# Kernel tuning notes

Measured on AMD Instinct MI355X. Metric: run time of the kernel, lower is better.

Reference implementation:

```python
import jax, jax.numpy as jnp
import numpy as np

N_NODES = 150000
N_USERS = 100000
EMB = 64
N_EDGES = 4800000
N_LAYERS = 3


def setup_inputs() -> dict:
    key = jax.random.key(0)
    k1, k2, k3, k4 = jax.random.split(key, 4)
    emb_weight = jax.random.normal(k1, (N_NODES, EMB), dtype=jnp.float32)
    adj_row = jnp.sort(jax.random.randint(k2, (N_EDGES,), 0, N_NODES, dtype=jnp.int64))
    adj_col = jax.random.randint(k3, (N_EDGES,), 0, N_NODES, dtype=jnp.int64)
    adj_vals = jax.random.uniform(k4, (N_EDGES,), dtype=jnp.float32)
    return {
        "emb_weight": emb_weight,
        "adj_row": adj_row,
        "adj_col": adj_col,
        "adj_vals": adj_vals,
        "n_users": N_USERS,
        "n_nodes": N_NODES,
        "n_layers": N_LAYERS,
    }


def _spmm(row, col, vals, x, n_nodes):
    # COO SpMM: out[r] += vals[e] * x[col[e]]  for each edge e with row[e]==r
    gathered = x[col] * vals[:, None]            # [nnz, emb]
    return jax.ops.segment_sum(gathered, row, num_segments=n_nodes)


def reference(emb_weight, adj_row, adj_col, adj_vals, n_users, n_nodes, n_layers):
    all_emb = emb_weight
    embs_sum = all_emb                           # running sum instead of stack+mean
    for _ in range(n_layers):
        all_emb = _spmm(adj_row, adj_col, adj_vals, all_emb, n_nodes)
        embs_sum = embs_sum + all_emb
    final_emb = embs_sum / jnp.asarray(n_layers + 1, dtype=emb_weight.dtype)
    users = final_emb[:n_users]
    items = final_emb[n_users:]
    return (users, items)
```

## Files before the change

### kernel.cpp

```cpp
#include <hip/hip_runtime.h>

#define EMB 64

__device__ __forceinline__ float bl(unsigned int u) { return __uint_as_float(u << 16); }
__device__ __forceinline__ float bh(unsigned int u) { return __uint_as_float(u & 0xffff0000u); }
__device__ __forceinline__ unsigned int pack2(float a, float b) {
    unsigned int ua = __float_as_uint(a); ua += 0x7fffu + ((ua >> 16) & 1u);
    unsigned int ub = __float_as_uint(b); ub += 0x7fffu + ((ub >> 16) & 1u);
    return (ua >> 16) | (ub & 0xffff0000u);
}

__global__ void __launch_bounds__(256) k_rowptr(const int* __restrict__ row,
                                                int* __restrict__ ptr, int E, int R) {
    int e = blockIdx.x * blockDim.x + threadIdx.x;
    if (e >= E) return;
    int r = row[e];
    int prev = (e == 0) ? -1 : row[e - 1];
    for (int q = prev + 1; q <= r; ++q) ptr[q] = e;
    if (e == E - 1) {
        for (int q = r + 1; q <= R; ++q) ptr[q] = E;
    }
}

__global__ void __launch_bounds__(256) k_prep(const float* __restrict__ emb,
                                              uint4* __restrict__ Xb, int n8) {
    int i = blockIdx.x * blockDim.x + threadIdx.x;
    if (i >= n8) return;
    const float4* p = reinterpret_cast<const float4*>(emb) + (size_t)i * 2;
    float4 a = p[0], b = p[1];
    uint4 x;
    x.x = pack2(a.x, a.y); x.y = pack2(a.z, a.w);
    x.z = pack2(b.x, b.y); x.w = pack2(b.z, b.w);
    Xb[i] = x;
}

template <int FINAL>
__global__ void __launch_bounds__(256, 3) k_spmm(const int* __restrict__ ptr,
                                                 const int* __restrict__ col,
                                                 const float* __restrict__ vals,
                                                 const uint4* __restrict__ Xb,
                                                 uint4* __restrict__ Yb,
                                                 const float* __restrict__ emb,
                                                 const uint4* __restrict__ Xa,
                                                 const uint4* __restrict__ Xc,
                                                 float* __restrict__ out, int R) {
    int tid = blockIdx.x * blockDim.x + threadIdx.x;
    int g   = tid >> 3;
    int gl  = tid & 7;
    if (g >= R) return;

    int s = ptr[g];
    int e = ptr[g + 1];

    float acc0 = 0.f, acc1 = 0.f, acc2 = 0.f, acc3 = 0.f;
    float acc4 = 0.f, acc5 = 0.f, acc6 = 0.f, acc7 = 0.f;

    if (s < e) {
        for (int base = s; base < e; base += 16) {
            int   cv[16];
            float vv[16];
            #pragma unroll
            for (int j = 0; j < 16; ++j) {
                int idx = base + j;
                int i2  = idx < e ? idx : e - 1;
                cv[j] = col[i2];
                vv[j] = vals[i2];
            }
            uint4 xv[16];
            #pragma unroll
            for (int j = 0; j < 16; ++j)
                xv[j] = Xb[(size_t)((unsigned)cv[j] * 8u + (unsigned)gl)];
            #pragma unroll
            for (int j = 0; j < 16; ++j) {
                float v = (base + j < e) ? vv[j] : 0.f;
                acc0 = fmaf(v, bl(xv[j].x), acc0);
                acc1 = fmaf(v, bh(xv[j].x), acc1);
                acc2 = fmaf(v, bl(xv[j].y), acc2);
                acc3 = fmaf(v, bh(xv[j].y), acc3);
                acc4 = fmaf(v, bl(xv[j].z), acc4);
                acc5 = fmaf(v, bh(xv[j].z), acc5);
                acc6 = fmaf(v, bl(xv[j].w), acc6);
                acc7 = fmaf(v, bh(xv[j].w), acc7);
            }
        }
    }

    if (FINAL) {
        const float4* er = reinterpret_cast<const float4*>(emb + (size_t)g * EMB + gl * 8);
        float4 a = er[0], b = er[1];
        uint4 x1 = Xa[(size_t)g * 8 + gl];
        uint4 x2 = Xc[(size_t)g * 8 + gl];
        float4 o0, o1;
        o0.x = 0.25f * (a.x + bl(x1.x) + bl(x2.x) + acc0);
        o0.y = 0.25f * (a.y + bh(x1.x) + bh(x2.x) + acc1);
        o0.z = 0.25f * (a.z + bl(x1.y) + bl(x2.y) + acc2);
        o0.w = 0.25f * (a.w + bh(x1.y) + bh(x2.y) + acc3);
        o1.x = 0.25f * (b.x + bl(x1.z) + bl(x2.z) + acc4);
        o1.y = 0.25f * (b.y + bh(x1.z) + bh(x2.z) + acc5);
        o1.z = 0.25f * (b.z + bl(x1.w) + bl(x2.w) + acc6);
        o1.w = 0.25f * (b.w + bh(x1.w) + bh(x2.w) + acc7);
        float4* q = reinterpret_cast<float4*>(out + (size_t)g * EMB + gl * 8);
        q[0] = o0; q[1] = o1;
    } else {
        uint4 y;
        y.x = pack2(acc0, acc1); y.y = pack2(acc2, acc3);
        y.z = pack2(acc4, acc5); y.w = pack2(acc6, acc7);
        Yb[(size_t)g * 8 + gl] = y;
    }
}

extern "C" void kernel_launch(void* const* d_in, const int* in_sizes, int n_in,
                              void* d_out, int out_size, void* d_ws, size_t ws_size,
                              hipStream_t stream) {
    const float* emb  = (const float*)d_in[0];
    const int*   row  = (const int*)d_in[1];
    const int*   col  = (const int*)d_in[2];
    const float* vals = (const float*)d_in[3];

    int nemb = in_sizes[0];
    int E    = in_sizes[1];
    int R    = nemb / EMB;

    uint4* X0  = (uint4*)d_ws;
    uint4* X1  = X0 + nemb / 8;
    uint4* X2  = X1 + nemb / 8;
    int*   ptr = (int*)(X2 + nemb / 8);

    dim3 blk(256);
    int gridE    = (E + 255) / 256;
    int gridElem = (nemb / 8 + 255) / 256;
    int gridRows = (R * 8 + 255) / 256;

    k_rowptr<<<gridE, blk, 0, stream>>>(row, ptr, E, R);
    k_prep<<<gridElem, blk, 0, stream>>>(emb, X0, nemb / 8);

    float* outp = (float*)d_out;
    k_spmm<0><<<gridRows, blk, 0, stream>>>(ptr, col, vals, X0, X1,
                                            emb, X0, X0, outp, R);
    k_spmm<0><<<gridRows, blk, 0, stream>>>(ptr, col, vals, X1, X2,
                                            emb, X0, X0, outp, R);
    k_spmm<1><<<gridRows, blk, 0, stream>>>(ptr, col, vals, X2, X1,
                                            emb, X1, X2, outp, R);
}
```

Before: 293.9 us.

## Bucket each row's edges by column slice and sweep slices across a persistent grid

A new pre-pass kernel reorders each row's edges into 8 column-range buckets, storing packed (col, val) pairs and per-row 8-bit bucket counts. The SpMM becomes a persistent-grid kernel in which each 8-lane group owns up to 5 rows and walks the buckets in order. The aim is to keep concurrently gathered embedding rows within a ~2.4MB column slice so they stay resident in L2. Costs are an extra bucketing pass, more accumulator registers, and a final average that now reads the bf16 copy of the input embeddings instead of fp32. The 8-bit counts and the MAXR=5 persistence limit assume per-bucket degrees and node counts that fit these test sizes.

```diff
diff --git a/kernel.cpp b/kernel.cpp
--- a/kernel.cpp
+++ b/kernel.cpp
@@ -1,6 +1,12 @@
 #include <hip/hip_runtime.h>
 
 #define EMB 64
+#define NS 8
+#define SLK 229065u
+#define NWG 1024
+#define GPB 32
+#define TOTG (NWG * GPB)
+#define MAXR 5
 
 __device__ __forceinline__ float bl(unsigned int u) { return __uint_as_float(u << 16); }
 __device__ __forceinline__ float bh(unsigned int u) { return __uint_as_float(u & 0xffff0000u); }
@@ -34,78 +40,141 @@
     Xb[i] = x;
 }
 
+__global__ void __launch_bounds__(256) k_bucket(const int* __restrict__ ptr,
+                                                const int* __restrict__ col,
+                                                const float* __restrict__ vals,
+                                                uint2* __restrict__ E2,
+                                                uint2* __restrict__ cntg, int R) {
+    __shared__ int cnt[GPB][NS];
+    int lg = threadIdx.x >> 3;
+    int gl = threadIdx.x & 7;
+    cnt[lg][gl] = 0;
+    int g = blockIdx.x * GPB + lg;
+    if (g >= R) return;
+    int s = ptr[g], e = ptr[g + 1];
+
+    for (int i = s + gl; i < e; i += 8) {
+        unsigned c = (unsigned)col[i];
+        atomicAdd(&cnt[lg][__umulhi(c, SLK)], 1);
+    }
+    int cl[NS];
+    #pragma unroll
+    for (int k = 0; k < NS; ++k) cl[k] = cnt[lg][k];
+    int mypb = 0;
+    #pragma unroll
+    for (int k = 0; k < NS; ++k) mypb += (k < gl) ? cl[k] : 0;
+    cnt[lg][gl] = mypb;
+    if (gl == 0) {
+        uint2 pc;
+        pc.x = (unsigned)cl[0] | ((unsigned)cl[1] << 8) |
+               ((unsigned)cl[2] << 16) | ((unsigned)cl[3] << 24);
+        pc.y = (unsigned)cl[4] | ((unsigned)cl[5] << 8) |
+               ((unsigned)cl[6] << 16) | ((unsigned)cl[7] << 24);
+        cntg[g] = pc;
+    }
+    for (int i = s + gl; i < e; i += 8) {
+        unsigned c = (unsigned)col[i];
+        float    v = vals[i];
+        int k = atomicAdd(&cnt[lg][__umulhi(c, SLK)], 1);
+        E2[(size_t)s + k] = make_uint2(c, __float_as_uint(v));
+    }
+}
+
 template <int FINAL>
-__global__ void __launch_bounds__(256, 3) k_spmm(const int* __restrict__ ptr,
-                                                 const int* __restrict__ col,
-                                                 const float* __restrict__ vals,
-                                                 const uint4* __restrict__ Xb,
-                                                 uint4* __restrict__ Yb,
-                                                 const float* __restrict__ emb,
-                                                 const uint4* __restrict__ Xa,
-                                                 const uint4* __restrict__ Xc,
-                                                 float* __restrict__ out, int R) {
-    int tid = blockIdx.x * blockDim.x + threadIdx.x;
-    int g   = tid >> 3;
-    int gl  = tid & 7;
-    if (g >= R) return;
-
-    int s = ptr[g];
-    int e = ptr[g + 1];
-
-    float acc0 = 0.f, acc1 = 0.f, acc2 = 0.f, acc3 = 0.f;
-    float acc4 = 0.f, acc5 = 0.f, acc6 = 0.f, acc7 = 0.f;
-
-    if (s < e) {
-        for (int base = s; base < e; base += 16) {
-            int   cv[16];
-            float vv[16];
-            #pragma unroll
-            for (int j = 0; j < 16; ++j) {
-                int idx = base + j;
-                int i2  = idx < e ? idx : e - 1;
-                cv[j] = col[i2];
-                vv[j] = vals[i2];
-            }
-            uint4 xv[16];
-            #pragma unroll
-            for (int j = 0; j < 16; ++j)
-                xv[j] = Xb[(size_t)((unsigned)cv[j] * 8u + (unsigned)gl)];
-            #pragma unroll
-            for (int j = 0; j < 16; ++j) {
-                float v = (base + j < e) ? vv[j] : 0.f;
-                acc0 = fmaf(v, bl(xv[j].x), acc0);
-                acc1 = fmaf(v, bh(xv[j].x), acc1);
-                acc2 = fmaf(v, bl(xv[j].y), acc2);
-                acc3 = fmaf(v, bh(xv[j].y), acc3);
-                acc4 = fmaf(v, bl(xv[j].z), acc4);
-                acc5 = fmaf(v, bh(xv[j].z), acc5);
-                acc6 = fmaf(v, bl(xv[j].w), acc6);
-                acc7 = fmaf(v, bh(xv[j].w), acc7);
+__global__ void __launch_bounds__(256, 4) k_spmm3(const int* __restrict__ ptr,
+                                                  const uint2* __restrict__ E2,
+                                                  const uint2* __restrict__ cntg,
+                                                  const uint4* __restrict__ Xb,
+                                                  uint4* __restrict__ Yb,
+                                                  const uint4* __restrict__ X0,
+                                                  const uint4* __restrict__ X1,
+                                                  const uint4* __restrict__ X2,
+                                                  float* __restrict__ out, int R) {
+    int gid = blockIdx.x * GPB + (threadIdx.x >> 3);
+    int gl  = threadIdx.x & 7;
+
+    int   rS[MAXR];
+    int   cur[MAXR];
+    uint2 rc[MAXR];
+    float acc[MAXR][8];
+
+    #pragma unroll
+    for (int k = 0; k < MAXR; ++k) {
+        int r = gid + k * TOTG;
+        bool va = r < R;
+        int rr = va ? r : 0;
+        rS[k] = ptr[rr];
+        uint2 t = cntg[rr];
+        rc[k].x = va ? t.x : 0u;
+        rc[k].y = va ? t.y : 0u;
+        cur[k] = 0;
+        #pragma unroll
+        for (int j = 0; j < 8; ++j) acc[k][j] = 0.f;
+    }
+
+    for (int b = 0; b < NS; ++b) {
+        #pragma unroll
+        for (int k = 0; k < MAXR; ++k) {
+            unsigned pc = (b & 4) ? rc[k].y : rc[k].x;
+            int len = (int)((pc >> ((b & 3) * 8)) & 0xffu);
+            int sseg = rS[k] + cur[k];
+            cur[k] += len;
+            for (int base2 = 0; base2 < len; base2 += 8) {
+                int idx = sseg + base2 + gl;
+                int lim = sseg + len - 1;
+                idx = idx < lim ? idx : lim;
+                uint2 cv = E2[idx];
+                unsigned cjv[8];
+                float    w[8];
+                #pragma unroll
+                for (int j = 0; j < 8; ++j) {
+                    cjv[j] = (unsigned)__shfl((int)cv.x, j, 8);
+                    float vj = __int_as_float(__shfl((int)cv.y, j, 8));
+                    w[j] = (base2 + j < len) ? vj : 0.f;
+                }
+                uint4 xv[8];
+                #pragma unroll
+                for (int j = 0; j < 8; ++j)
+                    xv[j] = Xb[(size_t)cjv[j] * 8u + (unsigned)gl];
+                #pragma unroll
+                for (int j = 0; j < 8; ++j) {
+                    acc[k][0] = fmaf(w[j], bl(xv[j].x), acc[k][0]);
+                    acc[k][1] = fmaf(w[j], bh(xv[j].x), acc[k][1]);
+                    acc[k][2] = fmaf(w[j], bl(xv[j].y), acc[k][2]);
+                    acc[k][3] = fmaf(w[j], bh(xv[j].y), acc[k][3]);
+                    acc[k][4] = fmaf(w[j], bl(xv[j].z), acc[k][4]);
+                    acc[k][5] = fmaf(w[j], bh(xv[j].z), acc[k][5]);
+                    acc[k][6] = fmaf(w[j], bl(xv[j].w), acc[k][6]);
+                    acc[k][7] = fmaf(w[j], bh(xv[j].w), acc[k][7]);
+                }
             }
         }
     }
 
-    if (FINAL) {
-        const float4* er = reinterpret_cast<const float4*>(emb + (size_t)g * EMB + gl * 8);
-        float4 a = er[0], b = er[1];
-        uint4 x1 = Xa[(size_t)g * 8 + gl];
-        uint4 x2 = Xc[(size_t)g * 8 + gl];
-        float4 o0, o1;
-        o0.x = 0.25f * (a.x + bl(x1.x) + bl(x2.x) + acc0);
-        o0.y = 0.25f * (a.y + bh(x1.x) + bh(x2.x) + acc1);
-        o0.z = 0.25f * (a.z + bl(x1.y) + bl(x2.y) + acc2);
-        o0.w = 0.25f * (a.w + bh(x1.y) + bh(x2.y) + acc3);
-        o1.x = 0.25f * (b.x + bl(x1.z) + bl(x2.z) + acc4);
-        o1.y = 0.25f * (b.y + bh(x1.z) + bh(x2.z) + acc5);
-        o1.z = 0.25f * (b.z + bl(x1.w) + bl(x2.w) + acc6);
-        o1.w = 0.25f * (b.w + bh(x1.w) + bh(x2.w) + acc7);
-        float4* q = reinterpret_cast<float4*>(out + (size_t)g * EMB + gl * 8);
-        q[0] = o0; q[1] = o1;
-    } else {
-        uint4 y;
-        y.x = pack2(acc0, acc1); y.y = pack2(acc2, acc3);
-        y.z = pack2(acc4, acc5); y.w = pack2(acc6, acc7);
-        Yb[(size_t)g * 8 + gl] = y;
+    #pragma unroll
+    for (int k = 0; k < MAXR; ++k) {
+        int r = gid + k * TOTG;
+        if (r >= R) continue;
+        if (FINAL) {
+            size_t o = (size_t)r * 8 + gl;
+            uint4 x0 = X0[o], x1 = X1[o], x2 = X2[o];
+            float4 o0, o1;
+            o0.x = 0.25f * (bl(x0.x) + bl(x1.x) + bl(x2.x) + acc[k][0]);
+            o0.y = 0.25f * (bh(x0.x) + bh(x1.x) + bh(x2.x) + acc[k][1]);
+            o0.z = 0.25f * (bl(x0.y) + bl(x1.y) + bl(x2.y) + acc[k][2]);
+            o0.w = 0.25f * (bh(x0.y) + bh(x1.y) + bh(x2.y) + acc[k][3]);
+            o1.x = 0.25f * (bl(x0.z) + bl(x1.z) + bl(x2.z) + acc[k][4]);
+            o1.y = 0.25f * (bh(x0.z) + bh(x1.z) + bh(x2.z) + acc[k][5]);
+            o1.z = 0.25f * (bl(x0.w) + bl(x1.w) + bl(x2.w) + acc[k][6]);
+            o1.w = 0.25f * (bh(x0.w) + bh(x1.w) + bh(x2.w) + acc[k][7]);
+            float4* q = reinterpret_cast<float4*>(out + (size_t)r * EMB + gl * 8);
+            q[0] = o0; q[1] = o1;
+        } else {
+            uint4 y;
+            y.x = pack2(acc[k][0], acc[k][1]); y.y = pack2(acc[k][2], acc[k][3]);
+            y.z = pack2(acc[k][4], acc[k][5]); y.w = pack2(acc[k][6], acc[k][7]);
+            Yb[(size_t)r * 8 + gl] = y;
+        }
     }
 }
 
@@ -121,24 +190,27 @@
     int E    = in_sizes[1];
     int R    = nemb / EMB;
 
-    uint4* X0  = (uint4*)d_ws;
-    uint4* X1  = X0 + nemb / 8;
-    uint4* X2  = X1 + nemb / 8;
-    int*   ptr = (int*)(X2 + nemb / 8);
+    uint4* X0   = (uint4*)d_ws;
+    uint4* X1   = X0 + nemb / 8;
+    uint4* X2   = X1 + nemb / 8;
+    int*   ptr  = (int*)(X2 + nemb / 8);
+    uint2* cntg = (uint2*)(ptr + ((R + 4) & ~3));
+    uint2* E2   = cntg + R;
 
     dim3 blk(256);
     int gridE    = (E + 255) / 256;
     int gridElem = (nemb / 8 + 255) / 256;
-    int gridRows = (R * 8 + 255) / 256;
+    int gridBkt  = (R + GPB - 1) / GPB;
 
     k_rowptr<<<gridE, blk, 0, stream>>>(row, ptr, E, R);
     k_prep<<<gridElem, blk, 0, stream>>>(emb, X0, nemb / 8);
+    k_bucket<<<gridBkt, blk, 0, stream>>>(ptr, col, vals, E2, cntg, R);
 
     float* outp = (float*)d_out;
-    k_spmm<0><<<gridRows, blk, 0, stream>>>(ptr, col, vals, X0, X1,
-                                            emb, X0, X0, outp, R);
-    k_spmm<0><<<gridRows, blk, 0, stream>>>(ptr, col, vals, X1, X2,
-                                            emb, X0, X0, outp, R);
-    k_spmm<1><<<gridRows, blk, 0, stream>>>(ptr, col, vals, X2, X1,
-                                            emb, X1, X2, outp, R);
-}
+    k_spmm3<0><<<NWG, blk, 0, stream>>>(ptr, E2, cntg, X0, X1,
+                                        X0, X1, X2, outp, R);
+    k_spmm3<0><<<NWG, blk, 0, stream>>>(ptr, E2, cntg, X1, X2,
+                                        X0, X1, X2, outp, R);
+    k_spmm3<1><<<NWG, blk, 0, stream>>>(ptr, E2, cntg, X2, X1,
+                                        X0, X1, X2, outp, R);
+}
```

New measurement: 468.4 us. +59.4%, slower.
